# Optimization experiments

Hardware: AMD Instinct MI355X
Metric: run time of the kernel (lower is better)

The kernel has to match this reference:

```python
import jax, jax.numpy as jnp
import numpy as np


def setup_inputs() -> dict:
    key = jax.random.key(0)
    kx, ka, kw, kb = jax.random.split(key, 4)
    B, N, IN, OUT = 4, 4096, 128, 128
    X = jax.random.normal(kx, (B, N, IN), dtype=jnp.float32)
    A = jax.random.uniform(ka, (B, N, N), dtype=jnp.float32)
    # nn.Linear(in_dim, out_dim): W is [out_dim, in_dim], b is [out_dim]
    bound = 1.0 / np.sqrt(IN)
    W = jax.random.uniform(kw, (OUT, IN), dtype=jnp.float32, minval=-bound, maxval=bound)
    b = jax.random.uniform(kb, (OUT,), dtype=jnp.float32, minval=-bound, maxval=bound)
    return {"X": X, "A": A, "W": W, "b": b}


def reference(X, A, W, b):
    B, N, _ = X.shape
    # A_hat = A + I (self loops)
    A_hat = A + jnp.eye(N, dtype=A.dtype)[None, :, :]
    deg = A_hat.sum(-1)  # [B, N]
    d_inv_sqrt = jnp.where(deg > 0, jax.lax.rsqrt(deg), 0.0)  # inf -> 0 as in torch code
    # D^{-1/2} A_hat D^{-1/2}: diag bmms are row/col scaling (same math, no N^3 diag GEMMs)
    A_norm = d_inv_sqrt[:, :, None] * A_hat * d_inv_sqrt[:, None, :]
    H = jnp.einsum('bnm,bmd->bnd', A_norm, X)  # propagation
    return jnp.einsum('bnd,od->bno', H, W) + b  # linear
```

## Files before the change

kernel.cpp:

```cpp
#include <hip/hip_runtime.h>
#include <hip/hip_bf16.h>
#include <stdint.h>

#define BB 4
#define NN 4096
#define DD 128

typedef __attribute__((ext_vector_type(8))) short short8;
typedef __attribute__((ext_vector_type(4))) float f32x4;

static __device__ __forceinline__ unsigned short f2bf(float f) {
  unsigned u = __builtin_bit_cast(unsigned, f);
  u += 0x7fffu + ((u >> 16) & 1u);
  return (unsigned short)(u >> 16);
}
static __device__ __forceinline__ float bf2f(unsigned short s) {
  return __builtin_bit_cast(float, (unsigned)s << 16);
}

__global__ __launch_bounds__(256) void k_deg(const float* __restrict__ A,
                                             float* __restrict__ dinv) {
  const int row = blockIdx.x;
  const float* a = A + (size_t)row * NN;
  float s = 0.f;
  for (int i = threadIdx.x * 4; i < NN; i += 256 * 4) {
    const float4 v = *reinterpret_cast<const float4*>(a + i);
    s += (v.x + v.y) + (v.z + v.w);
  }
  for (int off = 32; off > 0; off >>= 1) s += __shfl_down(s, off, 64);
  __shared__ float red[4];
  if ((threadIdx.x & 63) == 0) red[threadIdx.x >> 6] = s;
  __syncthreads();
  if (threadIdx.x == 0) {
    const float deg = (red[0] + red[1]) + (red[2] + red[3]) + 1.0f;
    dinv[row] = 1.0f / sqrtf(deg);
  }
}

__global__ __launch_bounds__(256) void k_prep(const float* __restrict__ X,
                                              const float* __restrict__ dinv,
                                              unsigned short* __restrict__ Yt,
                                              unsigned short* __restrict__ Yr)
{
  __shared__ unsigned short tile[64][130];
  const int b = blockIdx.x >> 6;
  const int m0 = (blockIdx.x & 63) << 6;
  const float* Xb = X + ((size_t)b * NN + m0) * DD;
  const float* dv = dinv + b * NN + m0;
  for (int idx = threadIdx.x; idx < 64 * 128; idx += 256) {
    const int mi = idx >> 7, d = idx & 127;
    const unsigned short u = f2bf(Xb[mi * DD + d] * dv[mi]);
    tile[mi][d] = u;
    Yr[((size_t)b * NN + m0 + mi) * DD + d] = u;
  }
  __syncthreads();
  for (int idx = threadIdx.x; idx < 128 * 64; idx += 256) {
    const int d = idx >> 6, j = idx & 63;
    Yt[((size_t)b * DD + d) * NN + m0 + j] = tile[j][d];
  }
}

__global__ __launch_bounds__(256) void k_w(const float* __restrict__ W,
                                           unsigned short* __restrict__ Wb) {
  int idx = blockIdx.x * 1024 + threadIdx.x;
  for (int k = 0; k < 4; ++k, idx += 256) Wb[idx] = f2bf(W[idx]);
}

__global__ __launch_bounds__(512) void k_main(const float* __restrict__ A,
                                              const unsigned short* __restrict__ Yt,
                                              const unsigned short* __restrict__ Yr,
                                              const float* __restrict__ dinv,
                                              unsigned short* __restrict__ Hb) {
  __shared__ char lds[49152];

  const int tid = threadIdx.x;
  const int l   = tid & 63;
  const int wid = tid >> 6;
  const int b   = blockIdx.x >> 6;
  const int n0  = (blockIdx.x & 63) << 6;
  const int wr  = wid >> 2;
  const int wc  = wid & 3;

  const float* Ab = A + (size_t)(b * NN + n0) * NN;
  const unsigned short* Ytb = Yt + (size_t)b * DD * NN;

  const int ar0 = tid >> 4;
  const int ar1 = ar0 + 32;
  const int ac4 = (tid & 15) << 2;
  const int aw0 = ar0 * 128 + ((ac4 << 1) ^ ((ar0 & 7) << 4));
  const int aw1 = ar1 * 128 + ((ac4 << 1) ^ ((ar1 & 7) << 4));

  const int yr0 = tid >> 3;
  const int yr1 = yr0 + 64;
  const int yc  = (tid & 7) << 4;
  const int yw0 = yr0 * 128 + (yc ^ ((yr0 & 7) << 4));
  const int yw1 = yr1 * 128 + (yc ^ ((yr1 & 7) << 4));

  float4 ra0, ra1;
  uint4  ry0, ry1;

  auto LOAD = [&](int t) {
    ra0 = *reinterpret_cast<const float4*>(Ab + (size_t)ar0 * NN + t * 64 + ac4);
    ra1 = *reinterpret_cast<const float4*>(Ab + (size_t)ar1 * NN + t * 64 + ac4);
    ry0 = *reinterpret_cast<const uint4*>(Ytb + (size_t)yr0 * NN + t * 64 + (yc >> 1));
    ry1 = *reinterpret_cast<const uint4*>(Ytb + (size_t)yr1 * NN + t * 64 + (yc >> 1));
  };
  auto WRITE = [&](int nb) {
    char* As = lds + nb * 8192;
    char* Ys = lds + 16384 + nb * 16384;
    *reinterpret_cast<ushort4*>(As + aw0) =
        make_ushort4(f2bf(ra0.x), f2bf(ra0.y), f2bf(ra0.z), f2bf(ra0.w));
    *reinterpret_cast<ushort4*>(As + aw1) =
        make_ushort4(f2bf(ra1.x), f2bf(ra1.y), f2bf(ra1.z), f2bf(ra1.w));
    *reinterpret_cast<uint4*>(Ys + yw0) = ry0;
    *reinterpret_cast<uint4*>(Ys + yw1) = ry1;
  };

  f32x4 acc[2][2] = {};
  const int lrow = l & 15;
  const int lk16 = (l >> 4) << 4;

  const int arow0 = wr * 32 + lrow, arow1 = arow0 + 16;
  const int brow0 = wc * 32 + lrow, brow1 = brow0 + 16;
  const int abase0 = arow0 * 128, abase1 = arow1 * 128;
  const int bbase0 = brow0 * 128, bbase1 = brow1 * 128;
  const int amsk0 = (arow0 & 7) << 4, amsk1 = (arow1 & 7) << 4;
  const int bmsk0 = (brow0 & 7) << 4, bmsk1 = (brow1 & 7) << 4;

  LOAD(0);
  WRITE(0);
  __syncthreads();
  int cur = 0;
  const int NT = NN / 64;
  for (int t = 0; t < NT; ++t) {
    if (t + 1 < NT) LOAD(t + 1);
    const char* As_ = lds + cur * 8192;
    const char* Ys_ = lds + 16384 + cur * 16384;
#pragma unroll
    for (int ks = 0; ks < 2; ++ks) {
      const int kb = ks * 64 + lk16;
      const short8 a0 = *reinterpret_cast<const short8*>(As_ + abase0 + (kb ^ amsk0));
      const short8 a1 = *reinterpret_cast<const short8*>(As_ + abase1 + (kb ^ amsk1));
      const short8 b0 = *reinterpret_cast<const short8*>(Ys_ + bbase0 + (kb ^ bmsk0));
      const short8 b1 = *reinterpret_cast<const short8*>(Ys_ + bbase1 + (kb ^ bmsk1));
      acc[0][0] = __builtin_amdgcn_mfma_f32_16x16x32_bf16(a0, b0, acc[0][0], 0, 0, 0);
      acc[0][1] = __builtin_amdgcn_mfma_f32_16x16x32_bf16(a0, b1, acc[0][1], 0, 0, 0);
      acc[1][0] = __builtin_amdgcn_mfma_f32_16x16x32_bf16(a1, b0, acc[1][0], 0, 0, 0);
      acc[1][1] = __builtin_amdgcn_mfma_f32_16x16x32_bf16(a1, b1, acc[1][1], 0, 0, 0);
    }
    if (t + 1 < NT) WRITE(cur ^ 1);
    __syncthreads();
    cur ^= 1;
  }

  const int rg = (l >> 4) << 2;
#pragma unroll
  for (int mi = 0; mi < 2; ++mi)
#pragma unroll
    for (int ni = 0; ni < 2; ++ni)
#pragma unroll
      for (int r = 0; r < 4; ++r) {
        const int n = n0 + wr * 32 + mi * 16 + rg + r;
        const int d = wc * 32 + ni * 16 + lrow;
        const size_t gi = (size_t)(b * NN + n) * DD + d;
        const float h = (acc[mi][ni][r] + bf2f(Yr[gi])) * dinv[b * NN + n];
        Hb[gi] = f2bf(h);
      }
}

__global__ __launch_bounds__(512) void k_lin(const unsigned short* __restrict__ Hb,
                                             const unsigned short* __restrict__ Wb,
                                             const float* __restrict__ bias,
                                             float* __restrict__ out) {
  __shared__ char lds[49152];

  const int tid = threadIdx.x;
  const int l   = tid & 63;
  const int wid = tid >> 6;
  const int wr  = wid >> 2;
  const int wc  = wid & 3;
  const size_t r0 = (size_t)blockIdx.x * 64;

#pragma unroll
  for (int i = 0; i < 2; ++i) {
    const int c = tid + i * 512;
    const int row = c >> 4, colb = (c & 15) << 4;
    const uint4 v = *reinterpret_cast<const uint4*>(Hb + (r0 + row) * DD + (colb >> 1));
    *reinterpret_cast<uint4*>(lds + row * 256 + (colb ^ ((row & 7) << 4))) = v;
  }
#pragma unroll
  for (int i = 0; i < 4; ++i) {
    const int c = tid + i * 512;
    const int row = c >> 4, colb = (c & 15) << 4;
    const uint4 v = *reinterpret_cast<const uint4*>(Wb + row * DD + (colb >> 1));
    *reinterpret_cast<uint4*>(lds + 16384 + row * 256 + (colb ^ ((row & 7) << 4))) = v;
  }
  __syncthreads();

  f32x4 acc[2][2] = {};
  const int lrow = l & 15;
  const int lk16 = (l >> 4) << 4;
  const int arow0 = wr * 32 + lrow, arow1 = arow0 + 16;
  const int brow0 = wc * 32 + lrow, brow1 = brow0 + 16;
#pragma unroll
  for (int ks = 0; ks < 4; ++ks) {
    const int kb = ks * 64 + lk16;
    const short8 a0 = *reinterpret_cast<const short8*>(lds + arow0 * 256 + (kb ^ ((arow0 & 7) << 4)));
    const short8 a1 = *reinterpret_cast<const short8*>(lds + arow1 * 256 + (kb ^ ((arow1 & 7) << 4)));
    const short8 b0 = *reinterpret_cast<const short8*>(lds + 16384 + brow0 * 256 + (kb ^ ((brow0 & 7) << 4)));
    const short8 b1 = *reinterpret_cast<const short8*>(lds + 16384 + brow1 * 256 + (kb ^ ((brow1 & 7) << 4)));
    acc[0][0] = __builtin_amdgcn_mfma_f32_16x16x32_bf16(a0, b0, acc[0][0], 0, 0, 0);
    acc[0][1] = __builtin_amdgcn_mfma_f32_16x16x32_bf16(a0, b1, acc[0][1], 0, 0, 0);
    acc[1][0] = __builtin_amdgcn_mfma_f32_16x16x32_bf16(a1, b0, acc[1][0], 0, 0, 0);
    acc[1][1] = __builtin_amdgcn_mfma_f32_16x16x32_bf16(a1, b1, acc[1][1], 0, 0, 0);
  }

  const int rg = (l >> 4) << 2;
#pragma unroll
  for (int mi = 0; mi < 2; ++mi)
#pragma unroll
    for (int ni = 0; ni < 2; ++ni) {
      const int o = wc * 32 + ni * 16 + lrow;
      const float bo = bias[o];
#pragma unroll
      for (int r = 0; r < 4; ++r) {
        const int nloc = wr * 32 + mi * 16 + rg + r;
        out[(r0 + nloc) * DD + o] = acc[mi][ni][r] + bo;
      }
    }
}

extern "C" void kernel_launch(void* const* d_in, const int* in_sizes, int n_in,
                              void* d_out, int out_size, void* d_ws, size_t ws_size,
                              hipStream_t stream) {
  const float* X    = (const float*)d_in[0];
  const float* A    = (const float*)d_in[1];
  const float* W    = (const float*)d_in[2];
  const float* bias = (const float*)d_in[3];
  float* out = (float*)d_out;

  char* ws = (char*)d_ws;
  float* dinv = (float*)ws;
  unsigned short* Yt = (unsigned short*)(ws + 65536);
  unsigned short* Yr = Yt + (size_t)BB * DD * NN;
  unsigned short* Hb = Yr + (size_t)BB * NN * DD;
  unsigned short* Wb = Hb + (size_t)BB * NN * DD;

  k_deg <<<BB * NN, 256, 0, stream>>>(A, dinv);
  k_w   <<<16, 256, 0, stream>>>(W, Wb);
  k_prep<<<BB * (NN / 64), 256, 0, stream>>>(X, dinv, Yt, Yr);
  k_main<<<BB * (NN / 64), 512, 0, stream>>>(A, Yt, Yr, dinv, Hb);
  k_lin <<<(BB * NN) / 64, 512, 0, stream>>>(Hb, Wb, bias, out);
}
```

Baseline: 117.1 us.

## Load Y operand directly into registers and use one wave per row in degree kernel

The main GEMM kernel no longer stages the transposed Y tile through LDS. Each lane loads its MFMA B fragments straight from global memory into registers, double-buffered across an unrolled pair of iterations, which shrinks LDS from 48KB to 16KB and removes the Y LDS writes and reads. The degree kernel now assigns one wavefront per row, so the LDS reduction and block barrier are gone and the grid is a quarter the size. The cost is uncoalesced-ish 16-byte global loads of Y per lane, which may be repeated across waves that share the same columns.

Result: slower. 152.3 us (+30.1%).

```diff
diff --git a/kernel.cpp b/kernel.cpp
--- a/kernel.cpp
+++ b/kernel.cpp
@@ -20,21 +20,17 @@
 
 __global__ __launch_bounds__(256) void k_deg(const float* __restrict__ A,
                                              float* __restrict__ dinv) {
-  const int row = blockIdx.x;
+  const int w = threadIdx.x >> 6, l = threadIdx.x & 63;
+  const int row = blockIdx.x * 4 + w;
   const float* a = A + (size_t)row * NN;
   float s = 0.f;
-  for (int i = threadIdx.x * 4; i < NN; i += 256 * 4) {
-    const float4 v = *reinterpret_cast<const float4*>(a + i);
+#pragma unroll
+  for (int i = 0; i < 16; ++i) {
+    const float4 v = *reinterpret_cast<const float4*>(a + (i * 64 + l) * 4);
     s += (v.x + v.y) + (v.z + v.w);
   }
   for (int off = 32; off > 0; off >>= 1) s += __shfl_down(s, off, 64);
-  __shared__ float red[4];
-  if ((threadIdx.x & 63) == 0) red[threadIdx.x >> 6] = s;
-  __syncthreads();
-  if (threadIdx.x == 0) {
-    const float deg = (red[0] + red[1]) + (red[2] + red[3]) + 1.0f;
-    dinv[row] = 1.0f / sqrtf(deg);
-  }
+  if (l == 0) dinv[row] = 1.0f / sqrtf(s + 1.0f);
 }
 
 __global__ __launch_bounds__(256) void k_prep(const float* __restrict__ X,
@@ -71,7 +67,7 @@
                                               const unsigned short* __restrict__ Yr,
                                               const float* __restrict__ dinv,
                                               unsigned short* __restrict__ Hb) {
-  __shared__ char lds[49152];
+  __shared__ char lds[16384];
 
   const int tid = threadIdx.x;
   const int l   = tid & 63;
@@ -90,67 +86,77 @@
   const int aw0 = ar0 * 128 + ((ac4 << 1) ^ ((ar0 & 7) << 4));
   const int aw1 = ar1 * 128 + ((ac4 << 1) ^ ((ar1 & 7) << 4));
 
-  const int yr0 = tid >> 3;
-  const int yr1 = yr0 + 64;
-  const int yc  = (tid & 7) << 4;
-  const int yw0 = yr0 * 128 + (yc ^ ((yr0 & 7) << 4));
-  const int yw1 = yr1 * 128 + (yc ^ ((yr1 & 7) << 4));
+  const int lrow = l & 15;
+  const int lk8  = (l >> 4) << 3;
+  const int brow0 = wc * 32 + lrow, brow1 = brow0 + 16;
+  const unsigned short* pB0 = Ytb + (size_t)brow0 * NN + lk8;
+  const unsigned short* pB1 = Ytb + (size_t)brow1 * NN + lk8;
 
   float4 ra0, ra1;
-  uint4  ry0, ry1;
-
-  auto LOAD = [&](int t) {
+
+  auto LOADA = [&](int t) {
     ra0 = *reinterpret_cast<const float4*>(Ab + (size_t)ar0 * NN + t * 64 + ac4);
     ra1 = *reinterpret_cast<const float4*>(Ab + (size_t)ar1 * NN + t * 64 + ac4);
-    ry0 = *reinterpret_cast<const uint4*>(Ytb + (size_t)yr0 * NN + t * 64 + (yc >> 1));
-    ry1 = *reinterpret_cast<const uint4*>(Ytb + (size_t)yr1 * NN + t * 64 + (yc >> 1));
-  };
-  auto WRITE = [&](int nb) {
+  };
+  auto WRITEA = [&](int nb) {
     char* As = lds + nb * 8192;
-    char* Ys = lds + 16384 + nb * 16384;
     *reinterpret_cast<ushort4*>(As + aw0) =
         make_ushort4(f2bf(ra0.x), f2bf(ra0.y), f2bf(ra0.z), f2bf(ra0.w));
     *reinterpret_cast<ushort4*>(As + aw1) =
         make_ushort4(f2bf(ra1.x), f2bf(ra1.y), f2bf(ra1.z), f2bf(ra1.w));
-    *reinterpret_cast<uint4*>(Ys + yw0) = ry0;
-    *reinterpret_cast<uint4*>(Ys + yw1) = ry1;
+  };
+  auto LOADB = [&](int t, short8& b00, short8& b01, short8& b10, short8& b11) {
+    b00 = *reinterpret_cast<const short8*>(pB0 + t * 64);
+    b01 = *reinterpret_cast<const short8*>(pB0 + t * 64 + 32);
+    b10 = *reinterpret_cast<const short8*>(pB1 + t * 64);
+    b11 = *reinterpret_cast<const short8*>(pB1 + t * 64 + 32);
   };
 
   f32x4 acc[2][2] = {};
-  const int lrow = l & 15;
-  const int lk16 = (l >> 4) << 4;
-
   const int arow0 = wr * 32 + lrow, arow1 = arow0 + 16;
-  const int brow0 = wc * 32 + lrow, brow1 = brow0 + 16;
   const int abase0 = arow0 * 128, abase1 = arow1 * 128;
-  const int bbase0 = brow0 * 128, bbase1 = brow1 * 128;
   const int amsk0 = (arow0 & 7) << 4, amsk1 = (arow1 & 7) << 4;
-  const int bmsk0 = (brow0 & 7) << 4, bmsk1 = (brow1 & 7) << 4;
-
-  LOAD(0);
-  WRITE(0);
-  __syncthreads();
-  int cur = 0;
-  const int NT = NN / 64;
-  for (int t = 0; t < NT; ++t) {
-    if (t + 1 < NT) LOAD(t + 1);
-    const char* As_ = lds + cur * 8192;
-    const char* Ys_ = lds + 16384 + cur * 16384;
+  const int lk16 = lk8 << 1;
+
+  auto COMPUTE = [&](int nb, const short8& b00, const short8& b01,
+                     const short8& b10, const short8& b11) {
+    const char* As_ = lds + nb * 8192;
 #pragma unroll
     for (int ks = 0; ks < 2; ++ks) {
       const int kb = ks * 64 + lk16;
       const short8 a0 = *reinterpret_cast<const short8*>(As_ + abase0 + (kb ^ amsk0));
       const short8 a1 = *reinterpret_cast<const short8*>(As_ + abase1 + (kb ^ amsk1));
-      const short8 b0 = *reinterpret_cast<const short8*>(Ys_ + bbase0 + (kb ^ bmsk0));
-      const short8 b1 = *reinterpret_cast<const short8*>(Ys_ + bbase1 + (kb ^ bmsk1));
-      acc[0][0] = __builtin_amdgcn_mfma_f32_16x16x32_bf16(a0, b0, acc[0][0], 0, 0, 0);
-      acc[0][1] = __builtin_amdgcn_mfma_f32_16x16x32_bf16(a0, b1, acc[0][1], 0, 0, 0);
-      acc[1][0] = __builtin_amdgcn_mfma_f32_16x16x32_bf16(a1, b0, acc[1][0], 0, 0, 0);
-      acc[1][1] = __builtin_amdgcn_mfma_f32_16x16x32_bf16(a1, b1, acc[1][1], 0, 0, 0);
+      const short8 bb0 = ks ? b01 : b00;
+      const short8 bb1 = ks ? b11 : b10;
+      acc[0][0] = __builtin_amdgcn_mfma_f32_16x16x32_bf16(a0, bb0, acc[0][0], 0, 0, 0);
+      acc[0][1] = __builtin_amdgcn_mfma_f32_16x16x32_bf16(a0, bb1, acc[0][1], 0, 0, 0);
+      acc[1][0] = __builtin_amdgcn_mfma_f32_16x16x32_bf16(a1, bb0, acc[1][0], 0, 0, 0);
+      acc[1][1] = __builtin_amdgcn_mfma_f32_16x16x32_bf16(a1, bb1, acc[1][1], 0, 0, 0);
     }
-    if (t + 1 < NT) WRITE(cur ^ 1);
+  };
+
+  short8 e00, e01, e10, e11;
+  short8 o00, o01, o10, o11;
+
+  LOADA(0);
+  LOADB(0, e00, e01, e10, e11);
+  WRITEA(0);
+  __syncthreads();
+
+  const int NT = NN / 64;
+  for (int t = 0; t < NT; t += 2) {
+    LOADA(t + 1);
+    LOADB(t + 1, o00, o01, o10, o11);
+    COMPUTE(0, e00, e01, e10, e11);
+    WRITEA(1);
     __syncthreads();
-    cur ^= 1;
+    if (t + 2 < NT) {
+      LOADA(t + 2);
+      LOADB(t + 2, e00, e01, e10, e11);
+    }
+    COMPUTE(1, o00, o01, o10, o11);
+    if (t + 2 < NT) WRITEA(0);
+    __syncthreads();
   }
 
   const int rg = (l >> 4) << 2;
@@ -246,7 +252,7 @@
   unsigned short* Hb = Yr + (size_t)BB * NN * DD;
   unsigned short* Wb = Hb + (size_t)BB * NN * DD;
 
-  k_deg <<<BB * NN, 256, 0, stream>>>(A, dinv);
+  k_deg <<<BB * NN / 4, 256, 0, stream>>>(A, dinv);
   k_w   <<<16, 256, 0, stream>>>(W, Wb);
   k_prep<<<BB * (NN / 64), 256, 0, stream>>>(X, dinv, Yt, Yr);
   k_main<<<BB * (NN / 64), 512, 0, stream>>>(A, Yt, Yr, dinv, Hb);
```

## Stream Y tiles via global_load_lds and deepen A prefetch pipeline

Applied to the files above, without the earlier changes.

The bf16 Y operand is now copied from global memory straight into LDS with global_load_lds, so it no longer passes through registers. The A tile is still loaded and converted by threads, but prefetched two tiles ahead, and each thread writes a single 16-byte store instead of two 8-byte ones. Hand-placed s_waitcnt and raw s_barrier calls replace __syncthreads so that loads stay in flight across iterations. This aims to hide memory latency in the bandwidth-bound A stream, at the cost of fragile manual wait counts and possible LDS buffer hazards.

New measurement: 122.1 us. 4.3% more time.

```diff
diff --git a/kernel.cpp b/kernel.cpp
--- a/kernel.cpp
+++ b/kernel.cpp
@@ -84,76 +84,86 @@
   const float* Ab = A + (size_t)(b * NN + n0) * NN;
   const unsigned short* Ytb = Yt + (size_t)b * DD * NN;
 
-  const int ar0 = tid >> 4;
-  const int ar1 = ar0 + 32;
-  const int ac4 = (tid & 15) << 2;
-  const int aw0 = ar0 * 128 + ((ac4 << 1) ^ ((ar0 & 7) << 4));
-  const int aw1 = ar1 * 128 + ((ac4 << 1) ^ ((ar1 & 7) << 4));
-
-  const int yr0 = tid >> 3;
-  const int yr1 = yr0 + 64;
-  const int yc  = (tid & 7) << 4;
-  const int yw0 = yr0 * 128 + (yc ^ ((yr0 & 7) << 4));
-  const int yw1 = yr1 * 128 + (yc ^ ((yr1 & 7) << 4));
+  const int sar = tid >> 3;
+  const int sac = (tid & 7) << 3;
+  const float* pA = Ab + (size_t)sar * NN + sac;
+  const int awb = sar * 128 + (((tid & 7) << 4) ^ ((sar & 7) << 4));
+
+  const int brow_i0 = wid * 16 + (l >> 3);
+  const int bg      = ((l & 7) ^ (l >> 3)) << 3;
+  const char* pB0 = (const char*)(Ytb + (size_t)brow_i0 * NN + bg);
+  const char* pB1 = (const char*)(Ytb + (size_t)(brow_i0 + 8) * NN + bg);
 
   float4 ra0, ra1;
-  uint4  ry0, ry1;
-
-  auto LOAD = [&](int t) {
-    ra0 = *reinterpret_cast<const float4*>(Ab + (size_t)ar0 * NN + t * 64 + ac4);
-    ra1 = *reinterpret_cast<const float4*>(Ab + (size_t)ar1 * NN + t * 64 + ac4);
-    ry0 = *reinterpret_cast<const uint4*>(Ytb + (size_t)yr0 * NN + t * 64 + (yc >> 1));
-    ry1 = *reinterpret_cast<const uint4*>(Ytb + (size_t)yr1 * NN + t * 64 + (yc >> 1));
-  };
-  auto WRITE = [&](int nb) {
-    char* As = lds + nb * 8192;
-    char* Ys = lds + 16384 + nb * 16384;
-    *reinterpret_cast<ushort4*>(As + aw0) =
-        make_ushort4(f2bf(ra0.x), f2bf(ra0.y), f2bf(ra0.z), f2bf(ra0.w));
-    *reinterpret_cast<ushort4*>(As + aw1) =
-        make_ushort4(f2bf(ra1.x), f2bf(ra1.y), f2bf(ra1.z), f2bf(ra1.w));
-    *reinterpret_cast<uint4*>(Ys + yw0) = ry0;
-    *reinterpret_cast<uint4*>(Ys + yw1) = ry1;
+  auto LOADA = [&](int t) {
+    ra0 = *reinterpret_cast<const float4*>(pA + t * 64);
+    ra1 = *reinterpret_cast<const float4*>(pA + t * 64 + 4);
+  };
+  auto CVTWRITEA = [&](int nb) {
+    short8 v;
+    v[0] = (short)f2bf(ra0.x); v[1] = (short)f2bf(ra0.y);
+    v[2] = (short)f2bf(ra0.z); v[3] = (short)f2bf(ra0.w);
+    v[4] = (short)f2bf(ra1.x); v[5] = (short)f2bf(ra1.y);
+    v[6] = (short)f2bf(ra1.z); v[7] = (short)f2bf(ra1.w);
+    *reinterpret_cast<short8*>(lds + nb * 24576 + awb) = v;
+  };
+  auto GLDSB = [&](int t, int nb) {
+    char* dst = lds + nb * 24576 + 8192 + (wid * 2) * 1024;
+    __builtin_amdgcn_global_load_lds(pB0 + (size_t)t * 128, dst, 16, 0, 0);
+    __builtin_amdgcn_global_load_lds(pB1 + (size_t)t * 128, dst + 1024, 16, 0, 0);
   };
 
   f32x4 acc[2][2] = {};
   const int lrow = l & 15;
-  const int lk16 = (l >> 4) << 4;
-
-  const int arow0 = wr * 32 + lrow, arow1 = arow0 + 16;
-  const int brow0 = wc * 32 + lrow, brow1 = brow0 + 16;
-  const int abase0 = arow0 * 128, abase1 = arow1 * 128;
-  const int bbase0 = brow0 * 128, bbase1 = brow1 * 128;
-  const int amsk0 = (arow0 & 7) << 4, amsk1 = (arow1 & 7) << 4;
-  const int bmsk0 = (brow0 & 7) << 4, bmsk1 = (brow1 & 7) << 4;
-
-  LOAD(0);
-  WRITE(0);
-  __syncthreads();
-  int cur = 0;
-  const int NT = NN / 64;
-  for (int t = 0; t < NT; ++t) {
-    if (t + 1 < NT) LOAD(t + 1);
-    const char* As_ = lds + cur * 8192;
-    const char* Ys_ = lds + 16384 + cur * 16384;
-#pragma unroll
-    for (int ks = 0; ks < 2; ++ks) {
-      const int kb = ks * 64 + lk16;
-      const short8 a0 = *reinterpret_cast<const short8*>(As_ + abase0 + (kb ^ amsk0));
-      const short8 a1 = *reinterpret_cast<const short8*>(As_ + abase1 + (kb ^ amsk1));
-      const short8 b0 = *reinterpret_cast<const short8*>(Ys_ + bbase0 + (kb ^ bmsk0));
-      const short8 b1 = *reinterpret_cast<const short8*>(Ys_ + bbase1 + (kb ^ bmsk1));
+  const int lg   = l >> 4;
+  const int ar0 = wr * 32 + lrow, ar1 = ar0 + 16;
+  const int br0 = wc * 32 + lrow, br1 = br0 + 16;
+
+  auto COMPUTE = [&](int nb) {
+    const char* Abase = lds + nb * 24576;
+    const char* Bbase = Abase + 8192;
+#pragma unroll
+    for (int kc = 0; kc < 2; ++kc) {
+      const int g = kc * 4 + lg;
+      const short8 a0 = *reinterpret_cast<const short8*>(Abase + ar0 * 128 + ((g ^ (ar0 & 7)) << 4));
+      const short8 a1 = *reinterpret_cast<const short8*>(Abase + ar1 * 128 + ((g ^ (ar1 & 7)) << 4));
+      const short8 b0 = *reinterpret_cast<const short8*>(Bbase + br0 * 128 + ((g ^ (br0 & 7)) << 4));
+      const short8 b1 = *reinterpret_cast<const short8*>(Bbase + br1 * 128 + ((g ^ (br1 & 7)) << 4));
       acc[0][0] = __builtin_amdgcn_mfma_f32_16x16x32_bf16(a0, b0, acc[0][0], 0, 0, 0);
       acc[0][1] = __builtin_amdgcn_mfma_f32_16x16x32_bf16(a0, b1, acc[0][1], 0, 0, 0);
       acc[1][0] = __builtin_amdgcn_mfma_f32_16x16x32_bf16(a1, b0, acc[1][0], 0, 0, 0);
       acc[1][1] = __builtin_amdgcn_mfma_f32_16x16x32_bf16(a1, b1, acc[1][1], 0, 0, 0);
     }
-    if (t + 1 < NT) WRITE(cur ^ 1);
-    __syncthreads();
-    cur ^= 1;
-  }
-
-  const int rg = (l >> 4) << 2;
+  };
+
+  LOADA(0);
+  GLDSB(0, 0);
+  asm volatile("s_waitcnt vmcnt(2)" ::: "memory");
+  CVTWRITEA(0);
+  LOADA(1);
+  GLDSB(1, 1);
+  asm volatile("s_waitcnt vmcnt(4) lgkmcnt(0)" ::: "memory");
+  __builtin_amdgcn_s_barrier();
+
+  const int NT = NN / 64;
+  for (int t = 0; t < NT; ++t) {
+    COMPUTE(t & 1);
+    __builtin_amdgcn_s_barrier();
+    if (t + 1 < NT) {
+      asm volatile("s_waitcnt vmcnt(2)" ::: "memory");
+      CVTWRITEA((t + 1) & 1);
+      if (t + 2 < NT) {
+        LOADA(t + 2);
+        GLDSB(t + 2, t & 1);
+        asm volatile("s_waitcnt vmcnt(4) lgkmcnt(0)" ::: "memory");
+      } else {
+        asm volatile("s_waitcnt vmcnt(0) lgkmcnt(0)" ::: "memory");
+      }
+      __builtin_amdgcn_s_barrier();
+    }
+  }
+
+  const int rg = lg << 2;
 #pragma unroll
   for (int mi = 0; mi < 2; ++mi)
 #pragma unroll
```

## Reassociate linear layer before propagation and fuse bias into main GEMM epilogue

Applied to the files above, without the earlier changes.

The product is reassociated so that the scaled features are multiplied by W first, giving V = (D^-1/2 X) W^T. That result is stored transposed as bf16 for the big A-propagation GEMM, along with a float self-loop-plus-bias term. The main kernel then writes the final output directly, so the separate linear kernel and the intermediate H buffer go away. This removes one kernel launch and a round trip of H through memory. In exchange the small W GEMM moves into the prep kernel, and the result is rounded to bf16 before the large GEMM, which shifts rounding error.

Measured after the change: 118.8 us. About the same (+1.4%).

```diff
diff --git a/kernel.cpp b/kernel.cpp
--- a/kernel.cpp
+++ b/kernel.cpp
@@ -13,9 +13,6 @@
   unsigned u = __builtin_bit_cast(unsigned, f);
   u += 0x7fffu + ((u >> 16) & 1u);
   return (unsigned short)(u >> 16);
-}
-static __device__ __forceinline__ float bf2f(unsigned short s) {
-  return __builtin_bit_cast(float, (unsigned)s << 16);
 }
 
 __global__ __launch_bounds__(256) void k_deg(const float* __restrict__ A,
@@ -37,40 +34,114 @@
   }
 }
 
-__global__ __launch_bounds__(256) void k_prep(const float* __restrict__ X,
-                                              const float* __restrict__ dinv,
-                                              unsigned short* __restrict__ Yt,
-                                              unsigned short* __restrict__ Yr)
-{
-  __shared__ unsigned short tile[64][130];
-  const int b = blockIdx.x >> 6;
-  const int m0 = (blockIdx.x & 63) << 6;
-  const float* Xb = X + ((size_t)b * NN + m0) * DD;
-  const float* dv = dinv + b * NN + m0;
-  for (int idx = threadIdx.x; idx < 64 * 128; idx += 256) {
-    const int mi = idx >> 7, d = idx & 127;
-    const unsigned short u = f2bf(Xb[mi * DD + d] * dv[mi]);
-    tile[mi][d] = u;
-    Yr[((size_t)b * NN + m0 + mi) * DD + d] = u;
-  }
-  __syncthreads();
-  for (int idx = threadIdx.x; idx < 128 * 64; idx += 256) {
-    const int d = idx >> 6, j = idx & 63;
-    Yt[((size_t)b * DD + d) * NN + m0 + j] = tile[j][d];
-  }
-}
-
 __global__ __launch_bounds__(256) void k_w(const float* __restrict__ W,
                                            unsigned short* __restrict__ Wb) {
   int idx = blockIdx.x * 1024 + threadIdx.x;
   for (int k = 0; k < 4; ++k, idx += 256) Wb[idx] = f2bf(W[idx]);
 }
 
+__global__ __launch_bounds__(256) void k_zv(const float* __restrict__ X,
+                                            const float* __restrict__ dinv,
+                                            const unsigned short* __restrict__ Wb,
+                                            const float* __restrict__ bias,
+                                            unsigned short* __restrict__ Vt,
+                                            float* __restrict__ Vr2) {
+  __shared__ char lds[65792];
+  unsigned short* vt = (unsigned short*)(lds + 49152);
+
+  const int tid = threadIdx.x;
+  const int l   = tid & 63;
+  const int wid = tid >> 6;
+  const int b   = blockIdx.x >> 6;
+  const int m0  = (blockIdx.x & 63) << 6;
+  const float* Xb  = X + ((size_t)b * NN + m0) * DD;
+  const float* dvb = dinv + b * NN + m0;
+
+  {
+    const int row = tid >> 2;
+    const int cb  = (tid & 3) * 32;
+    const float dv = dvb[row];
+    char* Ys = lds + row * 256;
+#pragma unroll
+    for (int j = 0; j < 4; ++j) {
+      const float4 v0 = *reinterpret_cast<const float4*>(Xb + row * DD + cb + j * 8);
+      const float4 v1 = *reinterpret_cast<const float4*>(Xb + row * DD + cb + j * 8 + 4);
+      short8 v;
+      v[0] = (short)f2bf(v0.x * dv); v[1] = (short)f2bf(v0.y * dv);
+      v[2] = (short)f2bf(v0.z * dv); v[3] = (short)f2bf(v0.w * dv);
+      v[4] = (short)f2bf(v1.x * dv); v[5] = (short)f2bf(v1.y * dv);
+      v[6] = (short)f2bf(v1.z * dv); v[7] = (short)f2bf(v1.w * dv);
+      const int g = (tid & 3) * 4 + j;
+      *reinterpret_cast<short8*>(Ys + ((g ^ (row & 15)) << 4)) = v;
+    }
+  }
+  {
+    const int row = tid >> 1;
+    const int gb  = (tid & 1) * 8;
+    char* Ws = lds + 16384 + row * 256;
+#pragma unroll
+    for (int j = 0; j < 8; ++j) {
+      const uint4 v = *reinterpret_cast<const uint4*>(Wb + row * DD + (gb + j) * 8);
+      *reinterpret_cast<uint4*>(Ws + (((gb + j) ^ (row & 15)) << 4)) = v;
+    }
+  }
+  __syncthreads();
+
+  const int lrow = l & 15, lg = l >> 4;
+  const int wr = wid >> 1, wc = wid & 1;
+  const int ar0 = wr * 32 + lrow, ar1 = ar0 + 16;
+  f32x4 acc[2][4] = {};
+#pragma unroll
+  for (int kc = 0; kc < 4; ++kc) {
+    const int g = kc * 4 + lg;
+    const short8 a0 = *reinterpret_cast<const short8*>(lds + ar0 * 256 + ((g ^ (ar0 & 15)) << 4));
+    const short8 a1 = *reinterpret_cast<const short8*>(lds + ar1 * 256 + ((g ^ (ar1 & 15)) << 4));
+#pragma unroll
+    for (int ni = 0; ni < 4; ++ni) {
+      const int br = wc * 64 + ni * 16 + lrow;
+      const short8 bb = *reinterpret_cast<const short8*>(lds + 16384 + br * 256 + ((g ^ (br & 15)) << 4));
+      acc[0][ni] = __builtin_amdgcn_mfma_f32_16x16x32_bf16(a0, bb, acc[0][ni], 0, 0, 0);
+      acc[1][ni] = __builtin_amdgcn_mfma_f32_16x16x32_bf16(a1, bb, acc[1][ni], 0, 0, 0);
+    }
+  }
+
+  const int rg = lg << 2;
+#pragma unroll
+  for (int mi = 0; mi < 2; ++mi)
+#pragma unroll
+    for (int r = 0; r < 4; ++r) {
+      const int ml = wr * 32 + mi * 16 + rg + r;
+      const float dm = dvb[ml];
+#pragma unroll
+      for (int ni = 0; ni < 4; ++ni) {
+        const int o = wc * 64 + ni * 16 + lrow;
+        const float z = acc[mi][ni][r];
+        vt[ml * 130 + o] = f2bf(z);
+        Vr2[((size_t)(b * NN + m0 + ml)) * DD + o] = dm * z + bias[o];
+      }
+    }
+  __syncthreads();
+
+  {
+    const int o = tid >> 1, mc = (tid & 1) * 32;
+    unsigned w[16];
+#pragma unroll
+    for (int j = 0; j < 16; ++j)
+      w[j] = (unsigned)vt[(mc + 2 * j) * 130 + o] | ((unsigned)vt[(mc + 2 * j + 1) * 130 + o] << 16);
+    unsigned short* dst = Vt + ((size_t)b * DD + o) * NN + m0 + mc;
+#pragma unroll
+    for (int q = 0; q < 4; ++q) {
+      uint4 u; u.x = w[q*4]; u.y = w[q*4+1]; u.z = w[q*4+2]; u.w = w[q*4+3];
+      *reinterpret_cast<uint4*>(dst + q * 8) = u;
+    }
+  }
+}
+
 __global__ __launch_bounds__(512) void k_main(const float* __restrict__ A,
-                                              const unsigned short* __restrict__ Yt,
-                                              const unsigned short* __restrict__ Yr,
+                                              const unsigned short* __restrict__ Vt,
+                                              const float* __restrict__ Vr2,
                                               const float* __restrict__ dinv,
-                                              unsigned short* __restrict__ Hb) {
+                                              float* __restrict__ out) {
   __shared__ char lds[49152];
 
   const int tid = threadIdx.x;
@@ -82,13 +153,13 @@
   const int wc  = wid & 3;
 
   const float* Ab = A + (size_t)(b * NN + n0) * NN;
-  const unsigned short* Ytb = Yt + (size_t)b * DD * NN;
-
-  const int ar0 = tid >> 4;
-  const int ar1 = ar0 + 32;
-  const int ac4 = (tid & 15) << 2;
-  const int aw0 = ar0 * 128 + ((ac4 << 1) ^ ((ar0 & 7) << 4));
-  const int aw1 = ar1 * 128 + ((ac4 << 1) ^ ((ar1 & 7) << 4));
+  const unsigned short* Vtb = Vt + (size_t)b * DD * NN;
+
+  const int sar0 = tid >> 4;
+  const int sar1 = sar0 + 32;
+  const int ac4  = (tid & 15) << 2;
+  const int aw0  = sar0 * 128 + ((ac4 << 1) ^ ((sar0 & 7) << 4));
+  const int aw1  = sar1 * 128 + ((ac4 << 1) ^ ((sar1 & 7) << 4));
 
   const int yr0 = tid >> 3;
   const int yr1 = yr0 + 64;
@@ -100,10 +171,10 @@
   uint4  ry0, ry1;
 
   auto LOAD = [&](int t) {
-    ra0 = *reinterpret_cast<const float4*>(Ab + (size_t)ar0 * NN + t * 64 + ac4);
-    ra1 = *reinterpret_cast<const float4*>(Ab + (size_t)ar1 * NN + t * 64 + ac4);
-    ry0 = *reinterpret_cast<const uint4*>(Ytb + (size_t)yr0 * NN + t * 64 + (yc >> 1));
-    ry1 = *reinterpret_cast<const uint4*>(Ytb + (size_t)yr1 * NN + t * 64 + (yc >> 1));
+    ra0 = *reinterpret_cast<const float4*>(Ab + (size_t)sar0 * NN + t * 64 + ac4);
+    ra1 = *reinterpret_cast<const float4*>(Ab + (size_t)sar1 * NN + t * 64 + ac4);
+    ry0 = *reinterpret_cast<const uint4*>(Vtb + (size_t)yr0 * NN + t * 64 + (yc >> 1));
+    ry1 = *reinterpret_cast<const uint4*>(Vtb + (size_t)yr1 * NN + t * 64 + (yc >> 1));
   };
   auto WRITE = [&](int nb) {
     char* As = lds + nb * 8192;
@@ -157,75 +228,14 @@
 #pragma unroll
   for (int mi = 0; mi < 2; ++mi)
 #pragma unroll
-    for (int ni = 0; ni < 2; ++ni)
-#pragma unroll
-      for (int r = 0; r < 4; ++r) {
-        const int n = n0 + wr * 32 + mi * 16 + rg + r;
-        const int d = wc * 32 + ni * 16 + lrow;
-        const size_t gi = (size_t)(b * NN + n) * DD + d;
-        const float h = (acc[mi][ni][r] + bf2f(Yr[gi])) * dinv[b * NN + n];
-        Hb[gi] = f2bf(h);
-      }
-}
-
-__global__ __launch_bounds__(512) void k_lin(const unsigned short* __restrict__ Hb,
-                                             const unsigned short* __restrict__ Wb,
-                                             const float* __restrict__ bias,
-                                             float* __restrict__ out) {
-  __shared__ char lds[49152];
-
-  const int tid = threadIdx.x;
-  const int l   = tid & 63;
-  const int wid = tid >> 6;
-  const int wr  = wid >> 2;
-  const int wc  = wid & 3;
-  const size_t r0 = (size_t)blockIdx.x * 64;
-
-#pragma unroll
-  for (int i = 0; i < 2; ++i) {
-    const int c = tid + i * 512;
-    const int row = c >> 4, colb = (c & 15) << 4;
-    const uint4 v = *reinterpret_cast<const uint4*>(Hb + (r0 + row) * DD + (colb >> 1));
-    *reinterpret_cast<uint4*>(lds + row * 256 + (colb ^ ((row & 7) << 4))) = v;
-  }
-#pragma unroll
-  for (int i = 0; i < 4; ++i) {
-    const int c = tid + i * 512;
-    const int row = c >> 4, colb = (c & 15) << 4;
-    const uint4 v = *reinterpret_cast<const uint4*>(Wb + row * DD + (colb >> 1));
-    *reinterpret_cast<uint4*>(lds + 16384 + row * 256 + (colb ^ ((row & 7) << 4))) = v;
-  }
-  __syncthreads();
-
-  f32x4 acc[2][2] = {};
-  const int lrow = l & 15;
-  const int lk16 = (l >> 4) << 4;
-  const int arow0 = wr * 32 + lrow, arow1 = arow0 + 16;
-  const int brow0 = wc * 32 + lrow, brow1 = brow0 + 16;
-#pragma unroll
-  for (int ks = 0; ks < 4; ++ks) {
-    const int kb = ks * 64 + lk16;
-    const short8 a0 = *reinterpret_cast<const short8*>(lds + arow0 * 256 + (kb ^ ((arow0 & 7) << 4)));
-    const short8 a1 = *reinterpret_cast<const short8*>(lds + arow1 * 256 + (kb ^ ((arow1 & 7) << 4)));
-    const short8 b0 = *reinterpret_cast<const short8*>(lds + 16384 + brow0 * 256 + (kb ^ ((brow0 & 7) << 4)));
-    const short8 b1 = *reinterpret_cast<const short8*>(lds + 16384 + brow1 * 256 + (kb ^ ((brow1 & 7) << 4)));
-    acc[0][0] = __builtin_amdgcn_mfma_f32_16x16x32_bf16(a0, b0, acc[0][0], 0, 0, 0);
-    acc[0][1] = __builtin_amdgcn_mfma_f32_16x16x32_bf16(a0, b1, acc[0][1], 0, 0, 0);
-    acc[1][0] = __builtin_amdgcn_mfma_f32_16x16x32_bf16(a1, b0, acc[1][0], 0, 0, 0);
-    acc[1][1] = __builtin_amdgcn_mfma_f32_16x16x32_bf16(a1, b1, acc[1][1], 0, 0, 0);
-  }
-
-  const int rg = (l >> 4) << 2;
-#pragma unroll
-  for (int mi = 0; mi < 2; ++mi)
-#pragma unroll
-    for (int ni = 0; ni < 2; ++ni) {
-      const int o = wc * 32 + ni * 16 + lrow;
-      const float bo = bias[o];
-#pragma unroll
-      for (int r = 0; r < 4; ++r) {
-        const int nloc = wr * 32 + mi * 16 + rg + r;
-        out[(r0 + nloc) * DD + o] = acc[mi][ni][r] + bo;
+    for (int r = 0; r < 4; ++r) {
+      const int n = n0 + wr * 32 + mi * 16 + rg + r;
+      const float dn = dinv[b * NN + n];
+#pragma unroll
+      for (int ni = 0; ni < 2; ++ni) {
+        const int o = wc * 32 + ni * 16 + lrow;
+        const size_t gi = (size_t)(b * NN + n) * DD + o;
+        out[gi] = dn * acc[mi][ni][r] + Vr2[gi];
       }
     }
 }
@@ -241,14 +251,12 @@
 
   char* ws = (char*)d_ws;
   float* dinv = (float*)ws;
-  unsigned short* Yt = (unsigned short*)(ws + 65536);
-  unsigned short* Yr = Yt + (size_t)BB * DD * NN;
-  unsigned short* Hb = Yr + (size_t)BB * NN * DD;
-  unsigned short* Wb = Hb + (size_t)BB * NN * DD;
-
+  unsigned short* Wb = (unsigned short*)(ws + 65536);
+  unsigned short* Vt = Wb + 32768 / 2;
+  float* Vr2 = (float*)((char*)Vt + (size_t)BB * DD * NN * 2);
+
+  k_w   <<<16, 256, 0, stream>>>(W, Wb);
   k_deg <<<BB * NN, 256, 0, stream>>>(A, dinv);
-  k_w   <<<16, 256, 0, stream>>>(W, Wb);
-  k_prep<<<BB * (NN / 64), 256, 0, stream>>>(X, dinv, Yt, Yr);
-  k_main<<<BB * (NN / 64), 512, 0, stream>>>(A, Yt, Yr, dinv, Hb);
-  k_lin <<<(BB * NN) / 64, 512, 0, stream>>>(Hb, Wb, bias, out);
-}
+  k_zv  <<<BB * (NN / 64), 256, 0, stream>>>(X, dinv, Wb, bias, Vt, Vr2);
+  k_main<<<BB * (NN / 64), 512, 0, stream>>>(A, Vt, Vr2, dinv, out);
+}
```
